# Performance work log

Hardware: AMD Instinct MI355X
Metric: run time of the kernel (lower is better)

Reference implementation:

```python
import jax, jax.numpy as jnp
import numpy as np

B, C, L, D = 8, 256, 2048, 128  # batch, in_channels, seq_len, n_factor


def setup_inputs() -> dict:
    key = jax.random.key(0)
    ks = jax.random.split(key, 8)
    s = 1.0 / np.sqrt(C)
    return {
        "x_inner": jax.random.normal(ks[0], (B, C, L), jnp.float32),
        "x_outer": jax.random.normal(ks[1], (B, C, L), jnp.float32),
        "Wq": jax.random.normal(ks[2], (D, C), jnp.float32) * s,
        "bq": jax.random.normal(ks[3], (D,), jnp.float32) * 0.01,
        "Wk": jax.random.normal(ks[4], (D, C), jnp.float32) * s,
        "bk": jax.random.normal(ks[5], (D,), jnp.float32) * 0.01,
        "Wv": jax.random.normal(ks[6], (D, C), jnp.float32) * s,
        "bv": jax.random.normal(ks[7], (D,), jnp.float32) * 0.01,
    }


def reference(x_inner, x_outer, Wq, bq, Wk, bk, Wv, bv):
    # kernel-size-1 Conv1d == per-position linear over channels; permute -> [B, L, D]
    q = jnp.einsum('bcl,dc->bld', x_inner, Wq) + bq  # [B, Lq, D]
    k = jnp.einsum('bcl,dc->bld', x_outer, Wk) + bk  # [B, Lk, D]
    v = jnp.einsum('bcl,dc->bld', x_outer, Wv) + bv  # [B, Lk, D]
    scores = jnp.einsum('bqd,bkd->bqk', q, k) / jnp.sqrt(jnp.asarray(D, q.dtype))
    attn = jax.nn.softmax(scores, axis=2)            # [B, Lq, Lk]
    return jnp.einsum('bqk,bkd->bqd', attn, v)       # [B, Lq, D]
```

## Files before the change

kernel.cpp:

```cpp
#include <hip/hip_runtime.h>
#include <hip/hip_bf16.h>

#define NB 8
#define NC 256
#define NL 2048
#define ND 128
#define NROWS (NB * NL)
#define QKV_ELEMS ((size_t)NB * NL * ND)
#define W_ELEMS (ND * NC)
#define XS_STRIDE 264

typedef __attribute__((ext_vector_type(8))) short bf16x8;
typedef __attribute__((ext_vector_type(4))) float f32x4;
typedef __attribute__((ext_vector_type(16))) float f32x16;
typedef __attribute__((ext_vector_type(4))) unsigned int u32x4;

__device__ __forceinline__ unsigned short f2bf(float f) {
    union { float f; unsigned u; } v; v.f = f;
    unsigned r = v.u + 0x7fffu + ((v.u >> 16) & 1u);
    return (unsigned short)(r >> 16);
}

__device__ __forceinline__ unsigned cvt_pk_bf16(float lo, float hi) {
    unsigned r;
    asm("v_cvt_pk_bf16_f32 %0, %1, %2" : "=v"(r) : "v"(lo), "v"(hi));
    return r;
}

__device__ __forceinline__ void pl32swap(unsigned &a, unsigned &b) {
    asm("v_permlane32_swap_b32 %0, %1" : "+v"(a), "+v"(b));
}

__device__ __forceinline__ void load_lds16(const unsigned short* g, unsigned short* l) {
    __builtin_amdgcn_global_load_lds((const __attribute__((address_space(1))) unsigned int*)g,
                                     (__attribute__((address_space(3))) unsigned int*)l, 16, 0, 0);
}

__global__ void cast_w3(const float* __restrict__ wq, const float* __restrict__ wk,
                        const float* __restrict__ wv, unsigned short* __restrict__ dst) {
    int i = blockIdx.x * blockDim.x + threadIdx.x;
    if (i >= 3 * W_ELEMS) return;
    int sel = i / W_ELEMS, off = i - sel * W_ELEMS;
    const float* s = (sel == 0) ? wq : (sel == 1) ? wk : wv;
    dst[i] = f2bf(s[off]);
}

__global__ __launch_bounds__(256, 4) void proj_direct(const float* __restrict__ xi,
                                                      const float* __restrict__ xo,
                                                      const unsigned short* __restrict__ Wall,
                                                      const float* __restrict__ bq,
                                                      const float* __restrict__ bk,
                                                      const float* __restrict__ bv,
                                                      unsigned short* __restrict__ Qb,
                                                      unsigned short* __restrict__ Kb,
                                                      unsigned short* __restrict__ Vtb) {
    __shared__ unsigned short xs[64 * XS_STRIDE];
    int b = blockIdx.x >> 5, lt = blockIdx.x & 31, l0 = lt * 64;
    int y = blockIdx.y;
    int wave = threadIdx.x >> 6, lane = threadIdx.x & 63;
    int ln = lane & 15, quad = lane >> 4;

    const float* xsrc = (y == 0 ? xi : xo) + (size_t)b * NC * NL + l0;
    int l4 = (lane & 15) * 4;
    int cr0 = wave * 4 + (lane >> 4);
    #pragma unroll
    for (int g = 0; g < 4; g++) {
        float4 r[4];
        #pragma unroll
        for (int gi = 0; gi < 4; gi++) {
            int c = cr0 + (g * 4 + gi) * 16;
            r[gi] = *reinterpret_cast<const float4*>(xsrc + (size_t)c * NL + l4);
        }
        #pragma unroll
        for (int gi = 0; gi < 4; gi++) {
            int c = cr0 + (g * 4 + gi) * 16;
            xs[(l4 + 0) * XS_STRIDE + c] = f2bf(r[gi].x);
            xs[(l4 + 1) * XS_STRIDE + c] = f2bf(r[gi].y);
            xs[(l4 + 2) * XS_STRIDE + c] = f2bf(r[gi].z);
            xs[(l4 + 3) * XS_STRIDE + c] = f2bf(r[gi].w);
        }
    }
    __syncthreads();

    if (y < 2) {
        const unsigned short* Wb = Wall + (size_t)y * W_ELEMS;
        const float* bias = y ? bk : bq;
        unsigned short* out = y ? Kb : Qb;
        int m0w = wave * 16;
        f32x4 acc[8] = {};
        #pragma unroll
        for (int s = 0; s < 8; s++) {
            bf16x8 af = *reinterpret_cast<const bf16x8*>(xs + (m0w + ln) * XS_STRIDE + s * 32 + quad * 8);
            #pragma unroll
            for (int t = 0; t < 8; t++) {
                bf16x8 bfr = *reinterpret_cast<const bf16x8*>(Wb + (size_t)(t * 16 + ln) * NC + s * 32 + quad * 8);
                acc[t] = __builtin_amdgcn_mfma_f32_16x16x32_bf16(af, bfr, acc[t], 0, 0, 0);
            }
        }
        #pragma unroll
        for (int t = 0; t < 8; t++) {
            int col = t * 16 + ln;
            float bi = bias[col];
            #pragma unroll
            for (int r = 0; r < 4; r++)
                out[(size_t)(b * NL + l0 + m0w + quad * 4 + r) * ND + col] = f2bf(acc[t][r] + bi);
        }
    } else {
        const unsigned short* Wb = Wall + 2 * (size_t)W_ELEMS;
        f32x4 acc[2][4] = {};
        #pragma unroll
        for (int s = 0; s < 8; s++) {
            bf16x8 wf0 = *reinterpret_cast<const bf16x8*>(Wb + (size_t)(wave * 32 + ln) * NC + s * 32 + quad * 8);
            bf16x8 wf1 = *reinterpret_cast<const bf16x8*>(Wb + (size_t)(wave * 32 + 16 + ln) * NC + s * 32 + quad * 8);
            #pragma unroll
            for (int t = 0; t < 4; t++) {
                bf16x8 xb = *reinterpret_cast<const bf16x8*>(xs + (t * 16 + ln) * XS_STRIDE + s * 32 + quad * 8);
                acc[0][t] = __builtin_amdgcn_mfma_f32_16x16x32_bf16(wf0, xb, acc[0][t], 0, 0, 0);
                acc[1][t] = __builtin_amdgcn_mfma_f32_16x16x32_bf16(wf1, xb, acc[1][t], 0, 0, 0);
            }
        }
        #pragma unroll
        for (int u = 0; u < 2; u++)
            #pragma unroll
            for (int t = 0; t < 4; t++)
                #pragma unroll
                for (int r = 0; r < 4; r++) {
                    int d = wave * 32 + u * 16 + quad * 4 + r;
                    Vtb[(size_t)(b * ND + d) * NL + l0 + t * 16 + ln] = f2bf(acc[u][t][r] + bv[d]);
                }
    }
}

__global__ __launch_bounds__(256, 2) void flash_attn_split(const unsigned short* __restrict__ Q,
                                                           const unsigned short* __restrict__ K,
                                                           const unsigned short* __restrict__ Vt,
                                                           float* __restrict__ Opart,
                                                           float* __restrict__ lbuf,
                                                           int kvlen) {
    __shared__ unsigned short kbuf[2][64 * 128];
    __shared__ unsigned short vbuf[2][128 * 64];
    int bx = blockIdx.x;
    bx = ((bx & 7) << 4) | (bx >> 3);
    int b = bx >> 4, qt = bx & 15;
    int sp = blockIdx.y;
    int kv0 = sp * kvlen;
    int wave = threadIdx.x >> 6, lane = threadIdx.x & 63;
    int l31 = lane & 31, h = lane >> 5;
    int m0 = qt * 128 + wave * 32;
    const float scale = 0.08838834764831845f * 1.4426950408889634f;

    bf16x8 qf[8];
    const unsigned short* qrow = Q + (size_t)(b * NL + m0 + l31) * ND + h * 8;
    #pragma unroll
    for (int s = 0; s < 8; s++) qf[s] = *reinterpret_cast<const bf16x8*>(qrow + s * 16);

    float lsum = 0.f;
    f32x16 o_acc[4] = {};

    const unsigned short* kg = K + (size_t)b * NL * ND;
    const unsigned short* vg = Vt + (size_t)b * ND * NL;

    int krt = wave * 16 + (lane >> 4);
    int kjs = (lane & 15);
    int vdt = wave * 32 + (lane >> 3);
    int vjs = (lane & 7);

    {
        int kt = kv0;
        #pragma unroll
        for (int i = 0; i < 4; i++) {
            int rt = krt + i * 4;
            load_lds16(kg + (size_t)(kt + rt) * ND + (kjs ^ (rt & 15)) * 8, kbuf[0] + (wave * 16 + i * 4) * 128);
        }
        #pragma unroll
        for (int i = 0; i < 4; i++) {
            int dt = vdt + i * 8;
            load_lds16(vg + (size_t)dt * NL + kt + (vjs ^ (dt & 7)) * 8, vbuf[0] + (wave * 32 + i * 8) * 64);
        }
    }

    int niter = kvlen >> 6;
    for (int it = 0; it < niter; it++) {
        int cur = it & 1;
        __syncthreads();

        if (it + 1 < niter) {
            int kt = kv0 + (it + 1) * 64;
            int nxt = cur ^ 1;
            #pragma unroll
            for (int i = 0; i < 4; i++) {
                int rt = krt + i * 4;
                load_lds16(kg + (size_t)(kt + rt) * ND + (kjs ^ (rt & 15)) * 8, kbuf[nxt] + (wave * 16 + i * 4) * 128);
            }
            #pragma unroll
            for (int i = 0; i < 4; i++) {
                int dt = vdt + i * 8;
                load_lds16(vg + (size_t)dt * NL + kt + (vjs ^ (dt & 7)) * 8, vbuf[nxt] + (wave * 32 + i * 8) * 64);
            }
        }
        const unsigned short* kb = kbuf[cur];
        const unsigned short* vb = vbuf[cur];

        f32x16 sacc[2] = {};
        __builtin_amdgcn_s_setprio(1);
        #pragma unroll
        for (int tt = 0; tt < 2; tt++) {
            const unsigned short* krow_p = kb + (tt * 32 + l31) * 128;
            #pragma unroll
            for (int s = 0; s < 8; s++) {
                bf16x8 kf = *reinterpret_cast<const bf16x8*>(krow_p + (((s * 2 + h) ^ (lane & 15)) << 3));
                sacc[tt] = __builtin_amdgcn_mfma_f32_32x32x16_bf16(kf, qf[s], sacc[tt], 0, 0, 0);
            }
        }
        __builtin_amdgcn_s_setprio(0);

        bf16x8 pb[4];
        #pragma unroll
        for (int tt = 0; tt < 2; tt++) {
            float p[16];
            #pragma unroll
            for (int g = 0; g < 16; g++) p[g] = __builtin_exp2f(sacc[tt][g] * scale);
            lsum += (((p[0] + p[1]) + (p[2] + p[3])) + ((p[4] + p[5]) + (p[6] + p[7])))
                  + (((p[8] + p[9]) + (p[10] + p[11])) + ((p[12] + p[13]) + (p[14] + p[15])));
            unsigned c0 = cvt_pk_bf16(p[0], p[1]),   c1 = cvt_pk_bf16(p[2], p[3]);
            unsigned c2 = cvt_pk_bf16(p[4], p[5]),   c3 = cvt_pk_bf16(p[6], p[7]);
            unsigned c4 = cvt_pk_bf16(p[8], p[9]),   c5 = cvt_pk_bf16(p[10], p[11]);
            unsigned c6 = cvt_pk_bf16(p[12], p[13]), c7 = cvt_pk_bf16(p[14], p[15]);
            pl32swap(c0, c2); pl32swap(c1, c3);
            pl32swap(c4, c6); pl32swap(c5, c7);
            u32x4 wlo = {c0, c1, c2, c3};
            u32x4 whi = {c4, c5, c6, c7};
            pb[tt * 2]     = __builtin_bit_cast(bf16x8, wlo);
            pb[tt * 2 + 1] = __builtin_bit_cast(bf16x8, whi);
        }

        __builtin_amdgcn_s_setprio(1);
        #pragma unroll
        for (int dt = 0; dt < 4; dt++) {
            const unsigned short* vrow = vb + (dt * 32 + l31) * 64;
            #pragma unroll
            for (int step = 0; step < 4; step++) {
                bf16x8 vf = *reinterpret_cast<const bf16x8*>(vrow + (((step * 2 + h) ^ (l31 & 7)) << 3));
                o_acc[dt] = __builtin_amdgcn_mfma_f32_32x32x16_bf16(vf, pb[step], o_acc[dt], 0, 0, 0);
            }
        }
        __builtin_amdgcn_s_setprio(0);
    }
    lsum += __shfl_xor(lsum, 32);

    float* op = Opart + (size_t)sp * QKV_ELEMS;
    int qrow_g = b * NL + m0 + l31;
    if (lane < 32) lbuf[(size_t)sp * NROWS + qrow_g] = lsum;
    #pragma unroll
    for (int dt = 0; dt < 4; dt++) {
        #pragma unroll
        for (int g = 0; g < 4; g++) {
            f32x4 v4 = { o_acc[dt][g * 4 + 0], o_acc[dt][g * 4 + 1],
                         o_acc[dt][g * 4 + 2], o_acc[dt][g * 4 + 3] };
            *reinterpret_cast<f32x4*>(op + (size_t)qrow_g * ND + dt * 32 + g * 8 + h * 4) = v4;
        }
    }
}

__global__ __launch_bounds__(256) void attn_merge(const float* __restrict__ Opart,
                                                  const float* __restrict__ lbuf,
                                                  float* __restrict__ out, int S) {
    int idx = blockIdx.x * 256 + threadIdx.x;
    int row = idx >> 5;
    int dg = (idx & 31) * 4;
    float L = 0.f;
    float4 acc = make_float4(0.f, 0.f, 0.f, 0.f);
    for (int s = 0; s < S; s++) {
        L += lbuf[(size_t)s * NROWS + row];
        float4 o = *reinterpret_cast<const float4*>(Opart + (size_t)s * QKV_ELEMS + (size_t)row * ND + dg);
        acc.x += o.x; acc.y += o.y; acc.z += o.z; acc.w += o.w;
    }
    float inv = 1.0f / L;
    float4 res = make_float4(acc.x * inv, acc.y * inv, acc.z * inv, acc.w * inv);
    *reinterpret_cast<float4*>(out + (size_t)row * ND + dg) = res;
}

extern "C" void kernel_launch(void* const* d_in, const int* in_sizes, int n_in,
                              void* d_out, int out_size, void* d_ws, size_t ws_size,
                              hipStream_t stream) {
    const float* x_inner = (const float*)d_in[0];
    const float* x_outer = (const float*)d_in[1];
    const float* Wq = (const float*)d_in[2];
    const float* bq = (const float*)d_in[3];
    const float* Wk = (const float*)d_in[4];
    const float* bk = (const float*)d_in[5];
    const float* Wv = (const float*)d_in[6];
    const float* bv = (const float*)d_in[7];
    float* out = (float*)d_out;

    size_t need4 = 34078720u + 3 * QKV_ELEMS * 2 + 3 * W_ELEMS * 2;
    int S = (ws_size >= need4) ? 4 : 2;
    size_t union_bytes = (S == 4) ? 34078720u : 17039360u;

    char* w = (char*)d_ws;
    float* Opart = (float*)w;
    float* lbuf = (float*)(w + (size_t)S * QKV_ELEMS * 4);
    unsigned short* Qb = (unsigned short*)(w + union_bytes);
    unsigned short* Kb = Qb + QKV_ELEMS;
    unsigned short* Vtb = Kb + QKV_ELEMS;
    unsigned short* Wall = Vtb + QKV_ELEMS;

    cast_w3<<<(3 * W_ELEMS + 255) / 256, 256, 0, stream>>>(Wq, Wk, Wv, Wall);
    dim3 pgrid(NB * (NL / 64), 3);
    proj_direct<<<pgrid, 256, 0, stream>>>(x_inner, x_outer, Wall, bq, bk, bv, Qb, Kb, Vtb);
    dim3 fgrid(NB * (NL / 128), S);
    flash_attn_split<<<fgrid, 256, 0, stream>>>(Qb, Kb, Vtb, Opart, lbuf, NL / S);
    attn_merge<<<(NROWS * ND / 4 + 255) / 256, 256, 0, stream>>>(Opart, lbuf, out, S);
}
```

Measured before the change: 147.3 us.

## Fuse K and V projections per block and swizzle LDS transpose writes

The projection grid drops from three y-slices to two, so one block computes both K and V from a single staged copy of x_outer. This removes the duplicate global read and bf16 conversion of x_outer. The LDS staging now writes packed 4-channel bf16 pairs with an XOR column swizzle, replacing the scalar 16-bit stores, to cut bank conflicts; MFMA reads apply the same swizzle. The trade-off is that the y=1 blocks do twice the MFMA work, which unbalances them against the Q blocks.

```diff
diff --git a/kernel.cpp b/kernel.cpp
--- a/kernel.cpp
+++ b/kernel.cpp
@@ -43,6 +43,35 @@
     int sel = i / W_ELEMS, off = i - sel * W_ELEMS;
     const float* s = (sel == 0) ? wq : (sel == 1) ? wk : wv;
     dst[i] = f2bf(s[off]);
+}
+
+__device__ __forceinline__ int xs_col(int row, int col) {
+    return col ^ (((row >> 2) & 7) << 3);
+}
+
+__device__ __forceinline__ void qk_project(const unsigned short* xs, const unsigned short* Wb,
+                                           const float* bias, unsigned short* out,
+                                           int b, int l0, int wave, int ln, int quad) {
+    int m0w = wave * 16;
+    f32x4 acc[8] = {};
+    int rowq = m0w + ln;
+    #pragma unroll
+    for (int s = 0; s < 8; s++) {
+        bf16x8 af = *reinterpret_cast<const bf16x8*>(xs + rowq * XS_STRIDE + xs_col(rowq, s * 32 + quad * 8));
+        #pragma unroll
+        for (int t = 0; t < 8; t++) {
+            bf16x8 bfr = *reinterpret_cast<const bf16x8*>(Wb + (size_t)(t * 16 + ln) * NC + s * 32 + quad * 8);
+            acc[t] = __builtin_amdgcn_mfma_f32_16x16x32_bf16(af, bfr, acc[t], 0, 0, 0);
+        }
+    }
+    #pragma unroll
+    for (int t = 0; t < 8; t++) {
+        int col = t * 16 + ln;
+        float bi = bias[col];
+        #pragma unroll
+        for (int r = 0; r < 4; r++)
+            out[(size_t)(b * NL + l0 + m0w + quad * 4 + r) * ND + col] = f2bf(acc[t][r] + bi);
+    }
 }
 
 __global__ __launch_bounds__(256, 4) void proj_direct(const float* __restrict__ xi,
@@ -61,51 +90,31 @@
     int ln = lane & 15, quad = lane >> 4;
 
     const float* xsrc = (y == 0 ? xi : xo) + (size_t)b * NC * NL + l0;
-    int l4 = (lane & 15) * 4;
-    int cr0 = wave * 4 + (lane >> 4);
-    #pragma unroll
-    for (int g = 0; g < 4; g++) {
+    int l4 = ln * 4;
+    #pragma unroll
+    for (int G = 0; G < 4; G++) {
+        int c0 = G * 64 + wave * 16 + quad * 4;
         float4 r[4];
         #pragma unroll
-        for (int gi = 0; gi < 4; gi++) {
-            int c = cr0 + (g * 4 + gi) * 16;
-            r[gi] = *reinterpret_cast<const float4*>(xsrc + (size_t)c * NL + l4);
-        }
-        #pragma unroll
-        for (int gi = 0; gi < 4; gi++) {
-            int c = cr0 + (g * 4 + gi) * 16;
-            xs[(l4 + 0) * XS_STRIDE + c] = f2bf(r[gi].x);
-            xs[(l4 + 1) * XS_STRIDE + c] = f2bf(r[gi].y);
-            xs[(l4 + 2) * XS_STRIDE + c] = f2bf(r[gi].z);
-            xs[(l4 + 3) * XS_STRIDE + c] = f2bf(r[gi].w);
+        for (int cc = 0; cc < 4; cc++)
+            r[cc] = *reinterpret_cast<const float4*>(xsrc + (size_t)(c0 + cc) * NL + l4);
+        #pragma unroll
+        for (int k = 0; k < 4; k++) {
+            int row = l4 + k;
+            const float* f0 = reinterpret_cast<const float*>(&r[0]);
+            const float* f1 = reinterpret_cast<const float*>(&r[1]);
+            const float* f2 = reinterpret_cast<const float*>(&r[2]);
+            const float* f3 = reinterpret_cast<const float*>(&r[3]);
+            uint2 w2 = { cvt_pk_bf16(f0[k], f1[k]), cvt_pk_bf16(f2[k], f3[k]) };
+            *reinterpret_cast<uint2*>(&xs[row * XS_STRIDE + xs_col(row, c0)]) = w2;
         }
     }
     __syncthreads();
 
-    if (y < 2) {
-        const unsigned short* Wb = Wall + (size_t)y * W_ELEMS;
-        const float* bias = y ? bk : bq;
-        unsigned short* out = y ? Kb : Qb;
-        int m0w = wave * 16;
-        f32x4 acc[8] = {};
-        #pragma unroll
-        for (int s = 0; s < 8; s++) {
-            bf16x8 af = *reinterpret_cast<const bf16x8*>(xs + (m0w + ln) * XS_STRIDE + s * 32 + quad * 8);
-            #pragma unroll
-            for (int t = 0; t < 8; t++) {
-                bf16x8 bfr = *reinterpret_cast<const bf16x8*>(Wb + (size_t)(t * 16 + ln) * NC + s * 32 + quad * 8);
-                acc[t] = __builtin_amdgcn_mfma_f32_16x16x32_bf16(af, bfr, acc[t], 0, 0, 0);
-            }
-        }
-        #pragma unroll
-        for (int t = 0; t < 8; t++) {
-            int col = t * 16 + ln;
-            float bi = bias[col];
-            #pragma unroll
-            for (int r = 0; r < 4; r++)
-                out[(size_t)(b * NL + l0 + m0w + quad * 4 + r) * ND + col] = f2bf(acc[t][r] + bi);
-        }
+    if (y == 0) {
+        qk_project(xs, Wall, bq, Qb, b, l0, wave, ln, quad);
     } else {
+        qk_project(xs, Wall + W_ELEMS, bk, Kb, b, l0, wave, ln, quad);
         const unsigned short* Wb = Wall + 2 * (size_t)W_ELEMS;
         f32x4 acc[2][4] = {};
         #pragma unroll
@@ -114,7 +123,8 @@
             bf16x8 wf1 = *reinterpret_cast<const bf16x8*>(Wb + (size_t)(wave * 32 + 16 + ln) * NC + s * 32 + quad * 8);
             #pragma unroll
             for (int t = 0; t < 4; t++) {
-                bf16x8 xb = *reinterpret_cast<const bf16x8*>(xs + (t * 16 + ln) * XS_STRIDE + s * 32 + quad * 8);
+                int rowv = t * 16 + ln;
+                bf16x8 xb = *reinterpret_cast<const bf16x8*>(xs + rowv * XS_STRIDE + xs_col(rowv, s * 32 + quad * 8));
                 acc[0][t] = __builtin_amdgcn_mfma_f32_16x16x32_bf16(wf0, xb, acc[0][t], 0, 0, 0);
                 acc[1][t] = __builtin_amdgcn_mfma_f32_16x16x32_bf16(wf1, xb, acc[1][t], 0, 0, 0);
             }
@@ -306,7 +316,7 @@
     unsigned short* Wall = Vtb + QKV_ELEMS;
 
     cast_w3<<<(3 * W_ELEMS + 255) / 256, 256, 0, stream>>>(Wq, Wk, Wv, Wall);
-    dim3 pgrid(NB * (NL / 64), 3);
+    dim3 pgrid(NB * (NL / 64), 2);
     proj_direct<<<pgrid, 256, 0, stream>>>(x_inner, x_outer, Wall, bq, bk, bv, Qb, Kb, Vtb);
     dim3 fgrid(NB * (NL / 128), S);
     flash_attn_split<<<fgrid, 256, 0, stream>>>(Qb, Kb, Vtb, Opart, lbuf, NL / S);
```

Result: no change. 148.3 us (+0.7%).
